# Kernel optimization log

Hardware: AMD Instinct MI355X
Metric: run time of the kernel (lower is better)

Reference implementation:

```python
import jax, jax.numpy as jnp
import numpy as np


def setup_inputs() -> dict:
    key = jax.random.key(0)
    ks = jax.random.split(key, 8)
    B, L, D, N, DM = 2, 2048, 2048, 8, 1024
    return {
        "x": jax.random.normal(ks[0], (B, L, D), jnp.float32),
        "A_log": jax.random.normal(ks[1], (D, N), jnp.float32),
        "x_proj_w": jax.random.normal(ks[2], (2 * N, D), jnp.float32) * (D ** -0.5),
        "x_proj_b": jax.random.normal(ks[3], (2 * N,), jnp.float32) * 0.02,
        "dt_proj_w": jax.random.normal(ks[4], (D, D), jnp.float32) * (D ** -0.5),
        "dt_proj_b": jax.random.normal(ks[5], (D,), jnp.float32) * 0.02,
        "out_proj_w": jax.random.normal(ks[6], (DM, D), jnp.float32) * (D ** -0.5),
        "out_proj_b": jax.random.normal(ks[7], (DM,), jnp.float32) * 0.02,
    }


def reference(x, A_log, x_proj_w, x_proj_b, dt_proj_w, dt_proj_b, out_proj_w, out_proj_b):
    # x: (B, L, D);  A_log: (D, N)
    A = -jnp.exp(A_log)                                   # (D, N), negative -> stable decay
    x_dbl = x @ x_proj_w.T + x_proj_b                     # (B, L, 2N): per-token B_t, C_t
    Bm, Cm = jnp.split(x_dbl, 2, axis=-1)                 # each (B, L, N)
    dt = jax.nn.softplus(x @ dt_proj_w.T + dt_proj_b)     # (B, L, D) selective timestep

    Bsz, L, D = x.shape
    N = A_log.shape[1]

    def step(h, inp):
        dt_t, B_t, C_t, x_t = inp                         # (B,D),(B,N),(B,N),(B,D)
        dA = jnp.exp(dt_t[..., None] * A)                 # (B, D, N)
        dB = dt_t[..., None] * B_t[:, None, :]            # (B, D, N)
        h = dA * h + dB * x_t[..., None]                  # (B, D, N)
        y = jnp.einsum("bdn,bn->bd", h, C_t)              # (B, D)
        return h, y

    h0 = jnp.zeros((Bsz, D, N), x.dtype)
    xs = (dt.transpose(1, 0, 2), Bm.transpose(1, 0, 2),
          Cm.transpose(1, 0, 2), x.transpose(1, 0, 2))
    _, ys = jax.lax.scan(step, h0, xs)                    # ys: (L, B, D)
    y = ys.transpose(1, 0, 2)                             # (B, L, D)
    return y @ out_proj_w.T + out_proj_b                  # (B, L, d_model)
```

## Files before the change

### kernel.cpp

```cpp
#include <hip/hip_runtime.h>
#include <hip/hip_bf16.h>

constexpr int Bsz = 2;
constexpr int L   = 2048;
constexpr int D   = 2048;
constexpr int Nst = 8;
constexpr int DM  = 1024;
constexpr int M   = Bsz * L;

constexpr int CH  = 64;
constexpr int T   = L / CH;
constexpr int BDN = Bsz * D * Nst;

typedef __bf16 bf16x8 __attribute__((ext_vector_type(8)));
typedef float f32x4 __attribute__((ext_vector_type(4)));

__global__ void cvt_f32_bf16(const float* __restrict__ in, __bf16* __restrict__ out, int n4) {
    int i = blockIdx.x * blockDim.x + threadIdx.x;
    if (i >= n4) return;
    float4 v = reinterpret_cast<const float4*>(in)[i];
    union { __bf16 b[4]; ushort4 u; } cv;
    cv.b[0] = (__bf16)v.x; cv.b[1] = (__bf16)v.y; cv.b[2] = (__bf16)v.z; cv.b[3] = (__bf16)v.w;
    reinterpret_cast<ushort4*>(out)[i] = cv.u;
}

__global__ __launch_bounds__(256) void xdbl_kernel(
    const float* __restrict__ x, const float* __restrict__ w,
    const float* __restrict__ bias, float* __restrict__ xdbl,
    __bf16* __restrict__ x_bf)
{
    __shared__ float sw[16 * 2048];
    const int tid = threadIdx.x;
    for (int i = tid; i < 16 * 2048 / 4; i += 256)
        reinterpret_cast<float4*>(sw)[i] = reinterpret_cast<const float4*>(w)[i];
    __syncthreads();

    const int lane = tid & 63;
    const int wrow = tid >> 6;
    for (int rr = 0; rr < 4; ++rr) {
        const int row = blockIdx.x * 16 + wrow * 4 + rr;
        const float* xr = x + (size_t)row * D;
        __bf16* xb = x_bf + (size_t)row * D;
        float acc[16];
#pragma unroll
        for (int j = 0; j < 16; ++j) acc[j] = 0.f;
        for (int k = lane * 4; k < D; k += 256) {
            float4 xv = *reinterpret_cast<const float4*>(&xr[k]);
            union { __bf16 b[4]; ushort4 u; } cv;
            cv.b[0] = (__bf16)xv.x; cv.b[1] = (__bf16)xv.y;
            cv.b[2] = (__bf16)xv.z; cv.b[3] = (__bf16)xv.w;
            *reinterpret_cast<ushort4*>(&xb[k]) = cv.u;
#pragma unroll
            for (int j = 0; j < 16; ++j) {
                float4 wv = *reinterpret_cast<const float4*>(&sw[j * D + k]);
                acc[j] += xv.x * wv.x + xv.y * wv.y + xv.z * wv.z + xv.w * wv.w;
            }
        }
#pragma unroll
        for (int j = 0; j < 16; ++j) {
            float v = acc[j];
#pragma unroll
            for (int off = 32; off > 0; off >>= 1) v += __shfl_down(v, off, 64);
            if (lane == 0) xdbl[(size_t)row * 16 + j] = v + bias[j];
        }
    }
}

__device__ inline void async16(__bf16* lds, const __bf16* g) {
    __builtin_amdgcn_global_load_lds(
        (const __attribute__((address_space(1))) void*)g,
        (__attribute__((address_space(3))) void*)lds, 16, 0, 0);
}

template <int MODE>
__global__ __launch_bounds__(256, 2) void gemm_bt(
    const __bf16* __restrict__ A, const __bf16* __restrict__ Bw,
    const float* __restrict__ bias, float* __restrict__ C,
    int N, int K)
{
    constexpr int BM = 128, BN = 128, BK = 64;
    const int NT = K / BK;
    __shared__ __attribute__((aligned(16))) __bf16 lds[2][2][BM * BK];

    const int tid  = threadIdx.x;
    const int lane = tid & 63;
    const int wid  = tid >> 6;
    const int wm   = wid >> 1, wn = wid & 1;
    const int rowBase = blockIdx.y * BM;
    const int colBase = blockIdx.x * BN;
    const int lrow = lane & 15;
    const int kgrp = lane >> 4;

    float bv[4];
#pragma unroll
    for (int n = 0; n < 4; ++n) bv[n] = bias[colBase + wn * 64 + n * 16 + lrow];
    asm volatile("s_waitcnt vmcnt(0)" ::: "memory");

    const int trow = tid >> 3;
    const int scol = ((tid & 7) ^ (trow & 7)) * 8;
    const __bf16* gA[4]; const __bf16* gB[4];
#pragma unroll
    for (int ro = 0; ro < 4; ++ro) {
        gA[ro] = A  + (size_t)(rowBase + ro * 32 + trow) * K + scol;
        gB[ro] = Bw + (size_t)(colBase + ro * 32 + trow) * K + scol;
    }

    f32x4 acc[4][4];
#pragma unroll
    for (int i = 0; i < 4; ++i)
#pragma unroll
        for (int j = 0; j < 4; ++j) acc[i][j] = f32x4{0.f, 0.f, 0.f, 0.f};

    auto stage = [&](int kt, int bsel) {
        const int k0 = kt * BK;
#pragma unroll
        for (int ro = 0; ro < 4; ++ro) {
            async16(&lds[bsel][0][ro * 2048 + tid * 8], gA[ro] + k0);
            async16(&lds[bsel][1][ro * 2048 + tid * 8], gB[ro] + k0);
        }
    };

    stage(0, 0);
    stage(1, 1);

    for (int t = 0; t < NT; ++t) {
        if (t == NT - 1) asm volatile("s_waitcnt vmcnt(0)" ::: "memory");
        else             asm volatile("s_waitcnt vmcnt(8)" ::: "memory");
        __builtin_amdgcn_s_barrier();

        const int cur = t & 1;
        bf16x8 af[4][2], bfr[4][2];
#pragma unroll
        for (int m = 0; m < 4; ++m) {
            const int row = wm * 64 + m * 16 + lrow;
#pragma unroll
            for (int kk = 0; kk < 2; ++kk) {
                const int slot = (kk * 4 + kgrp) ^ (lrow & 7);
                af[m][kk] = *reinterpret_cast<const bf16x8*>(&lds[cur][0][row * 64 + slot * 8]);
            }
        }
#pragma unroll
        for (int n = 0; n < 4; ++n) {
            const int row = wn * 64 + n * 16 + lrow;
#pragma unroll
            for (int kk = 0; kk < 2; ++kk) {
                const int slot = (kk * 4 + kgrp) ^ (lrow & 7);
                bfr[n][kk] = *reinterpret_cast<const bf16x8*>(&lds[cur][1][row * 64 + slot * 8]);
            }
        }
        asm volatile("s_waitcnt lgkmcnt(0)" ::: "memory");
        __builtin_amdgcn_sched_barrier(0);
        __builtin_amdgcn_s_barrier();

        if (t + 2 < NT) stage(t + 2, cur);

        __builtin_amdgcn_s_setprio(1);
#pragma unroll
        for (int kk = 0; kk < 2; ++kk)
#pragma unroll
            for (int m = 0; m < 4; ++m)
#pragma unroll
                for (int n = 0; n < 4; ++n)
                    acc[m][n] = __builtin_amdgcn_mfma_f32_16x16x32_bf16(af[m][kk], bfr[n][kk], acc[m][n], 0, 0, 0);
        __builtin_amdgcn_s_setprio(0);
    }

#pragma unroll
    for (int m = 0; m < 4; ++m) {
        const int row = rowBase + wm * 64 + m * 16 + kgrp * 4;
#pragma unroll
        for (int n = 0; n < 4; ++n) {
            const int col = colBase + wn * 64 + n * 16 + lrow;
#pragma unroll
            for (int r = 0; r < 4; ++r) {
                float v = acc[m][n][r] + bv[n];
                if (MODE == 1) v = (v > 20.f) ? v : log1pf(expf(v));
                C[(size_t)(row + r) * N + col] = v;
            }
        }
    }
}

__global__ __launch_bounds__(64) void scan_p1(
    const float* __restrict__ dt, const float* __restrict__ x,
    const float* __restrict__ xdbl, const float* __restrict__ A_log,
    float* __restrict__ P, float* __restrict__ Hloc)
{
    const int tid = threadIdx.x;
    int blk = blockIdx.x;
    const int c  = blk % CH;  blk /= CH;
    const int dg = blk % (D / 64);
    const int b  = blk / (D / 64);
    const int d  = dg * 64 + tid;

    float A[Nst], h[Nst], p[Nst];
#pragma unroll
    for (int n = 0; n < Nst; ++n) {
        A[n] = -expf(A_log[(size_t)d * Nst + n]);
        h[n] = 0.f; p[n] = 1.f;
    }

    __shared__ __attribute__((aligned(16))) float sBC[T * 16];
    const float4* src = reinterpret_cast<const float4*>(xdbl + ((size_t)b * L + c * T) * 16);
#pragma unroll
    for (int i = tid; i < T * 4; i += 64)
        reinterpret_cast<float4*>(sBC)[i] = src[i];
    __syncthreads();

    const float* dt_p = dt + ((size_t)b * L + c * T) * D + d;
    const float* x_p  = x  + ((size_t)b * L + c * T) * D + d;
#pragma unroll 4
    for (int t2 = 0; t2 < T; ++t2) {
        const float dtv = dt_p[(size_t)t2 * D];
        const float xv  = x_p[(size_t)t2 * D];
        const float dtx = dtv * xv;
        const float* bc = &sBC[t2 * 16];
#pragma unroll
        for (int n = 0; n < Nst; ++n) {
            const float dA = __expf(dtv * A[n]);
            p[n] *= dA;
            h[n] = dA * h[n] + dtx * bc[n];
        }
    }
    const size_t base = ((size_t)c * Bsz * D + (size_t)b * D + d) * Nst;
#pragma unroll
    for (int n = 0; n < Nst; ++n) { P[base + n] = p[n]; Hloc[base + n] = h[n]; }
}

__global__ __launch_bounds__(256) void scan_p2(
    const float* __restrict__ P, const float* __restrict__ Hloc,
    float* __restrict__ Hstart)
{
    const int id = blockIdx.x * blockDim.x + threadIdx.x;
    if (id >= BDN) return;
    float h = 0.f;
    for (int c = 0; c < CH; ++c) {
        const size_t o = (size_t)c * BDN + id;
        Hstart[o] = h;
        h = P[o] * h + Hloc[o];
    }
}

__global__ __launch_bounds__(64) void scan_p3(
    const float* __restrict__ dt, const float* __restrict__ x,
    const float* __restrict__ xdbl, const float* __restrict__ A_log,
    const float* __restrict__ Hstart, __bf16* __restrict__ y_bf)
{
    const int tid = threadIdx.x;
    int blk = blockIdx.x;
    const int c  = blk % CH;  blk /= CH;
    const int dg = blk % (D / 64);
    const int b  = blk / (D / 64);
    const int d  = dg * 64 + tid;

    float A[Nst], h[Nst];
    const size_t hbase = ((size_t)c * Bsz * D + (size_t)b * D + d) * Nst;
#pragma unroll
    for (int n = 0; n < Nst; ++n) {
        A[n] = -expf(A_log[(size_t)d * Nst + n]);
        h[n] = Hstart[hbase + n];
    }

    __shared__ __attribute__((aligned(16))) float sBC[T * 16];
    const float4* src = reinterpret_cast<const float4*>(xdbl + ((size_t)b * L + c * T) * 16);
#pragma unroll
    for (int i = tid; i < T * 4; i += 64)
        reinterpret_cast<float4*>(sBC)[i] = src[i];
    __syncthreads();

    const float* dt_p = dt + ((size_t)b * L + c * T) * D + d;
    const float* x_p  = x  + ((size_t)b * L + c * T) * D + d;
    __bf16*      y_p  = y_bf + ((size_t)b * L + c * T) * D + d;
#pragma unroll 4
    for (int t2 = 0; t2 < T; ++t2) {
        const float dtv = dt_p[(size_t)t2 * D];
        const float xv  = x_p[(size_t)t2 * D];
        const float dtx = dtv * xv;
        const float* bc = &sBC[t2 * 16];
        float y = 0.f;
#pragma unroll
        for (int n = 0; n < Nst; ++n) {
            const float dA = __expf(dtv * A[n]);
            h[n] = dA * h[n] + dtx * bc[n];
            y = fmaf(h[n], bc[8 + n], y);
        }
        y_p[(size_t)t2 * D] = (__bf16)y;
    }
}

extern "C" void kernel_launch(void* const* d_in, const int* in_sizes, int n_in,
                              void* d_out, int out_size, void* d_ws, size_t ws_size,
                              hipStream_t stream) {
    const float* x     = (const float*)d_in[0];
    const float* A_log = (const float*)d_in[1];
    const float* xpw   = (const float*)d_in[2];
    const float* xpb   = (const float*)d_in[3];
    const float* dtw   = (const float*)d_in[4];
    const float* dtb   = (const float*)d_in[5];
    const float* ow    = (const float*)d_in[6];
    const float* ob    = (const float*)d_in[7];
    float* out = (float*)d_out;

    char* ws = (char*)d_ws;
    __bf16* x_bf   = (__bf16*)(ws);
    __bf16* dtw_bf = (__bf16*)(ws + 16777216);
    __bf16* ow_bf  = (__bf16*)(ws + 25165824);
    float*  xdbl   = (float* )(ws + 29360128);
    float*  dtbuf  = (float* )(ws + 29622272);
    __bf16* y_bf   = (__bf16*)(ws + 63176704);
    float*  P      = (float*)(ws);
    float*  Hloc   = (float*)(ws + 8388608);
    float*  Hstart = (float*)(ws + 16777216);

    cvt_f32_bf16<<<(D * D / 4 + 255) / 256, 256, 0, stream>>>(dtw, dtw_bf, D * D / 4);
    cvt_f32_bf16<<<(DM * D / 4 + 255) / 256, 256, 0, stream>>>(ow, ow_bf, DM * D / 4);

    xdbl_kernel<<<M / 16, 256, 0, stream>>>(x, xpw, xpb, xdbl, x_bf);

    gemm_bt<1><<<dim3(D / 128, M / 128), 256, 0, stream>>>(x_bf, dtw_bf, dtb, dtbuf, D, D);

    const int scan_blocks = Bsz * (D / 64) * CH;
    scan_p1<<<scan_blocks, 64, 0, stream>>>(dtbuf, x, xdbl, A_log, P, Hloc);
    scan_p2<<<(BDN + 255) / 256, 256, 0, stream>>>(P, Hloc, Hstart);
    scan_p3<<<scan_blocks, 64, 0, stream>>>(dtbuf, x, xdbl, A_log, Hstart, y_bf);

    gemm_bt<0><<<dim3(DM / 128, M / 128), 256, 0, stream>>>(y_bf, ow_bf, ob, out, DM, D);
}
```

Before: 185.8 us.

## Switch GEMM to 32x32x16 MFMA and split-K the output projection

Replaces the 16x16x32 bf16 MFMA tiles in the shared GEMM with 32x32x16 tiles, which changes the LDS fragment loads and the epilogue row mapping. The output projection GEMM (only 256 blocks) is also split along K into two z-slices that accumulate with atomic adds into a zero-initialised output, with the bias added only by the first slice. This aims to cut instruction-issue overhead and to fill more CUs for the small GEMM. In exchange it adds a memset, atomic traffic, and a summation order that is no longer deterministic.

```diff
diff --git a/kernel.cpp b/kernel.cpp
--- a/kernel.cpp
+++ b/kernel.cpp
@@ -13,7 +13,8 @@
 constexpr int BDN = Bsz * D * Nst;
 
 typedef __bf16 bf16x8 __attribute__((ext_vector_type(8)));
-typedef float f32x4 __attribute__((ext_vector_type(4)));
+typedef float f32x4  __attribute__((ext_vector_type(4)));
+typedef float f32x16 __attribute__((ext_vector_type(16)));
 
 __global__ void cvt_f32_bf16(const float* __restrict__ in, __bf16* __restrict__ out, int n4) {
     int i = blockIdx.x * blockDim.x + threadIdx.x;
@@ -76,10 +77,11 @@
 __global__ __launch_bounds__(256, 2) void gemm_bt(
     const __bf16* __restrict__ A, const __bf16* __restrict__ Bw,
     const float* __restrict__ bias, float* __restrict__ C,
-    int N, int K)
+    int N, int Kfull, int Ksub)
 {
     constexpr int BM = 128, BN = 128, BK = 64;
-    const int NT = K / BK;
+    const int NT  = Ksub / BK;
+    const int zoff = blockIdx.z * Ksub;
     __shared__ __attribute__((aligned(16))) __bf16 lds[2][2][BM * BK];
 
     const int tid  = threadIdx.x;
@@ -88,12 +90,16 @@
     const int wm   = wid >> 1, wn = wid & 1;
     const int rowBase = blockIdx.y * BM;
     const int colBase = blockIdx.x * BN;
-    const int lrow = lane & 15;
-    const int kgrp = lane >> 4;
-
-    float bv[4];
-#pragma unroll
-    for (int n = 0; n < 4; ++n) bv[n] = bias[colBase + wn * 64 + n * 16 + lrow];
+    const int l31   = lane & 31;
+    const int khalf = lane >> 5;
+    const int l7    = lane & 7;
+
+    float bv[2];
+#pragma unroll
+    for (int n = 0; n < 2; ++n) {
+        bv[n] = bias[colBase + wn * 64 + n * 32 + l31];
+        if (MODE == 2 && blockIdx.z != 0) bv[n] = 0.f;
+    }
     asm volatile("s_waitcnt vmcnt(0)" ::: "memory");
 
     const int trow = tid >> 3;
@@ -101,15 +107,17 @@
     const __bf16* gA[4]; const __bf16* gB[4];
 #pragma unroll
     for (int ro = 0; ro < 4; ++ro) {
-        gA[ro] = A  + (size_t)(rowBase + ro * 32 + trow) * K + scol;
-        gB[ro] = Bw + (size_t)(colBase + ro * 32 + trow) * K + scol;
-    }
-
-    f32x4 acc[4][4];
-#pragma unroll
-    for (int i = 0; i < 4; ++i)
-#pragma unroll
-        for (int j = 0; j < 4; ++j) acc[i][j] = f32x4{0.f, 0.f, 0.f, 0.f};
+        gA[ro] = A  + (size_t)(rowBase + ro * 32 + trow) * Kfull + zoff + scol;
+        gB[ro] = Bw + (size_t)(colBase + ro * 32 + trow) * Kfull + zoff + scol;
+    }
+
+    f32x16 acc[2][2];
+#pragma unroll
+    for (int i = 0; i < 2; ++i)
+#pragma unroll
+        for (int j = 0; j < 2; ++j)
+#pragma unroll
+            for (int r = 0; r < 16; ++r) acc[i][j][r] = 0.f;
 
     auto stage = [&](int kt, int bsel) {
         const int k0 = kt * BK;
@@ -129,23 +137,23 @@
         __builtin_amdgcn_s_barrier();
 
         const int cur = t & 1;
-        bf16x8 af[4][2], bfr[4][2];
-#pragma unroll
-        for (int m = 0; m < 4; ++m) {
-            const int row = wm * 64 + m * 16 + lrow;
-#pragma unroll
-            for (int kk = 0; kk < 2; ++kk) {
-                const int slot = (kk * 4 + kgrp) ^ (lrow & 7);
-                af[m][kk] = *reinterpret_cast<const bf16x8*>(&lds[cur][0][row * 64 + slot * 8]);
+        bf16x8 af[2][4], bfr[2][4];
+#pragma unroll
+        for (int m = 0; m < 2; ++m) {
+            const int row = wm * 64 + m * 32 + l31;
+#pragma unroll
+            for (int ks = 0; ks < 4; ++ks) {
+                const int slot = (ks * 2 + khalf) ^ l7;
+                af[m][ks] = *reinterpret_cast<const bf16x8*>(&lds[cur][0][row * 64 + slot * 8]);
             }
         }
 #pragma unroll
-        for (int n = 0; n < 4; ++n) {
-            const int row = wn * 64 + n * 16 + lrow;
-#pragma unroll
-            for (int kk = 0; kk < 2; ++kk) {
-                const int slot = (kk * 4 + kgrp) ^ (lrow & 7);
-                bfr[n][kk] = *reinterpret_cast<const bf16x8*>(&lds[cur][1][row * 64 + slot * 8]);
+        for (int n = 0; n < 2; ++n) {
+            const int row = wn * 64 + n * 32 + l31;
+#pragma unroll
+            for (int ks = 0; ks < 4; ++ks) {
+                const int slot = (ks * 2 + khalf) ^ l7;
+                bfr[n][ks] = *reinterpret_cast<const bf16x8*>(&lds[cur][1][row * 64 + slot * 8]);
             }
         }
         asm volatile("s_waitcnt lgkmcnt(0)" ::: "memory");
@@ -156,26 +164,28 @@
 
         __builtin_amdgcn_s_setprio(1);
 #pragma unroll
-        for (int kk = 0; kk < 2; ++kk)
-#pragma unroll
-            for (int m = 0; m < 4; ++m)
-#pragma unroll
-                for (int n = 0; n < 4; ++n)
-                    acc[m][n] = __builtin_amdgcn_mfma_f32_16x16x32_bf16(af[m][kk], bfr[n][kk], acc[m][n], 0, 0, 0);
+        for (int ks = 0; ks < 4; ++ks)
+#pragma unroll
+            for (int m = 0; m < 2; ++m)
+#pragma unroll
+                for (int n = 0; n < 2; ++n)
+                    acc[m][n] = __builtin_amdgcn_mfma_f32_32x32x16_bf16(af[m][ks], bfr[n][ks], acc[m][n], 0, 0, 0);
         __builtin_amdgcn_s_setprio(0);
     }
 
 #pragma unroll
-    for (int m = 0; m < 4; ++m) {
-        const int row = rowBase + wm * 64 + m * 16 + kgrp * 4;
-#pragma unroll
-        for (int n = 0; n < 4; ++n) {
-            const int col = colBase + wn * 64 + n * 16 + lrow;
-#pragma unroll
-            for (int r = 0; r < 4; ++r) {
+    for (int m = 0; m < 2; ++m) {
+        const int rb = rowBase + wm * 64 + m * 32 + 4 * khalf;
+#pragma unroll
+        for (int n = 0; n < 2; ++n) {
+            const int col = colBase + wn * 64 + n * 32 + l31;
+#pragma unroll
+            for (int r = 0; r < 16; ++r) {
+                const int row = rb + (r & 3) + 8 * (r >> 2);
                 float v = acc[m][n][r] + bv[n];
                 if (MODE == 1) v = (v > 20.f) ? v : log1pf(expf(v));
-                C[(size_t)(row + r) * N + col] = v;
+                if (MODE == 2) unsafeAtomicAdd(&C[(size_t)row * N + col], v);
+                else           C[(size_t)row * N + col] = v;
             }
         }
     }
@@ -317,12 +327,13 @@
 
     xdbl_kernel<<<M / 16, 256, 0, stream>>>(x, xpw, xpb, xdbl, x_bf);
 
-    gemm_bt<1><<<dim3(D / 128, M / 128), 256, 0, stream>>>(x_bf, dtw_bf, dtb, dtbuf, D, D);
+    gemm_bt<1><<<dim3(D / 128, M / 128, 1), 256, 0, stream>>>(x_bf, dtw_bf, dtb, dtbuf, D, D, D);
 
     const int scan_blocks = Bsz * (D / 64) * CH;
     scan_p1<<<scan_blocks, 64, 0, stream>>>(dtbuf, x, xdbl, A_log, P, Hloc);
     scan_p2<<<(BDN + 255) / 256, 256, 0, stream>>>(P, Hloc, Hstart);
     scan_p3<<<scan_blocks, 64, 0, stream>>>(dtbuf, x, xdbl, A_log, Hstart, y_bf);
 
-    gemm_bt<0><<<dim3(DM / 128, M / 128), 256, 0, stream>>>(y_bf, ow_bf, ob, out, DM, D);
-}
+    hipMemsetAsync(out, 0, (size_t)out_size * sizeof(float), stream);
+    gemm_bt<2><<<dim3(DM / 128, M / 128, 2), 256, 0, stream>>>(y_bf, ow_bf, ob, out, DM, D, D / 2);
+}
```

After: 212.9 us. 1.15x slower.

## Split-K the output projection GEMM and swizzle block order in dt GEMM

Applied to the files above, without the earlier changes.

The output projection GEMM is split along K into two halves via blockIdx.z, and each half writes partial results to a workspace buffer. A new reduce kernel then sums the two partials and adds the bias. This doubles the block count for the small-N GEMM (8x32 blocks) to fill more CUs, at the cost of extra partial-result traffic and one more launch. The dt GEMM also gets an XCD-style block-index swizzle, which groups tiles to improve L2 locality across chiplets.

```diff
diff --git a/kernel.cpp b/kernel.cpp
--- a/kernel.cpp
+++ b/kernel.cpp
@@ -13,7 +13,7 @@
 constexpr int BDN = Bsz * D * Nst;
 
 typedef __bf16 bf16x8 __attribute__((ext_vector_type(8)));
-typedef float f32x4 __attribute__((ext_vector_type(4)));
+typedef float f32x4  __attribute__((ext_vector_type(4)));
 
 __global__ void cvt_f32_bf16(const float* __restrict__ in, __bf16* __restrict__ out, int n4) {
     int i = blockIdx.x * blockDim.x + threadIdx.x;
@@ -72,28 +72,38 @@
         (__attribute__((address_space(3))) void*)lds, 16, 0, 0);
 }
 
-template <int MODE>
+template <int MODE, int SWZ>
 __global__ __launch_bounds__(256, 2) void gemm_bt(
     const __bf16* __restrict__ A, const __bf16* __restrict__ Bw,
     const float* __restrict__ bias, float* __restrict__ C,
-    int N, int K)
+    int N, int Kfull, int Ksub)
 {
     constexpr int BM = 128, BN = 128, BK = 64;
-    const int NT = K / BK;
+    const int NT  = Ksub / BK;
+    const int zoff = blockIdx.z * Ksub;
     __shared__ __attribute__((aligned(16))) __bf16 lds[2][2][BM * BK];
+
+    int bx = blockIdx.x, by = blockIdx.y;
+    if (SWZ) {
+        const int lin = by * gridDim.x + bx;
+        const int cpx = (gridDim.x * gridDim.y) >> 3;
+        const int swz = (lin & 7) * cpx + (lin >> 3);
+        bx = swz % gridDim.x; by = swz / gridDim.x;
+    }
 
     const int tid  = threadIdx.x;
     const int lane = tid & 63;
     const int wid  = tid >> 6;
     const int wm   = wid >> 1, wn = wid & 1;
-    const int rowBase = blockIdx.y * BM;
-    const int colBase = blockIdx.x * BN;
+    const int rowBase = by * BM;
+    const int colBase = bx * BN;
     const int lrow = lane & 15;
     const int kgrp = lane >> 4;
 
     float bv[4];
 #pragma unroll
-    for (int n = 0; n < 4; ++n) bv[n] = bias[colBase + wn * 64 + n * 16 + lrow];
+    for (int n = 0; n < 4; ++n)
+        bv[n] = (MODE == 3) ? 0.f : bias[colBase + wn * 64 + n * 16 + lrow];
     asm volatile("s_waitcnt vmcnt(0)" ::: "memory");
 
     const int trow = tid >> 3;
@@ -101,8 +111,8 @@
     const __bf16* gA[4]; const __bf16* gB[4];
 #pragma unroll
     for (int ro = 0; ro < 4; ++ro) {
-        gA[ro] = A  + (size_t)(rowBase + ro * 32 + trow) * K + scol;
-        gB[ro] = Bw + (size_t)(colBase + ro * 32 + trow) * K + scol;
+        gA[ro] = A  + (size_t)(rowBase + ro * 32 + trow) * Kfull + zoff + scol;
+        gB[ro] = Bw + (size_t)(colBase + ro * 32 + trow) * Kfull + zoff + scol;
     }
 
     f32x4 acc[4][4];
@@ -165,6 +175,7 @@
         __builtin_amdgcn_s_setprio(0);
     }
 
+    float* Cz = (MODE == 3) ? C + (size_t)blockIdx.z * M * N : C;
 #pragma unroll
     for (int m = 0; m < 4; ++m) {
         const int row = rowBase + wm * 64 + m * 16 + kgrp * 4;
@@ -175,10 +186,26 @@
             for (int r = 0; r < 4; ++r) {
                 float v = acc[m][n][r] + bv[n];
                 if (MODE == 1) v = (v > 20.f) ? v : log1pf(expf(v));
-                C[(size_t)(row + r) * N + col] = v;
+                Cz[(size_t)(row + r) * N + col] = v;
             }
         }
     }
+}
+
+__global__ __launch_bounds__(256) void reduce_bias(
+    const float* __restrict__ part, const float* __restrict__ bias,
+    float* __restrict__ out)
+{
+    const int i = blockIdx.x * blockDim.x + threadIdx.x;
+    const int n4 = M * DM / 4;
+    if (i >= n4) return;
+    float4 a = reinterpret_cast<const float4*>(part)[i];
+    float4 b = reinterpret_cast<const float4*>(part + (size_t)M * DM)[i];
+    float4 bb = *reinterpret_cast<const float4*>(&bias[(i * 4) % DM]);
+    float4 r;
+    r.x = a.x + b.x + bb.x; r.y = a.y + b.y + bb.y;
+    r.z = a.z + b.z + bb.z; r.w = a.w + b.w + bb.w;
+    reinterpret_cast<float4*>(out)[i] = r;
 }
 
 __global__ __launch_bounds__(64) void scan_p1(
@@ -311,18 +338,20 @@
     float*  P      = (float*)(ws);
     float*  Hloc   = (float*)(ws + 8388608);
     float*  Hstart = (float*)(ws + 16777216);
+    float*  Cpart  = (float*)(ws + 29622272);
 
     cvt_f32_bf16<<<(D * D / 4 + 255) / 256, 256, 0, stream>>>(dtw, dtw_bf, D * D / 4);
     cvt_f32_bf16<<<(DM * D / 4 + 255) / 256, 256, 0, stream>>>(ow, ow_bf, DM * D / 4);
 
     xdbl_kernel<<<M / 16, 256, 0, stream>>>(x, xpw, xpb, xdbl, x_bf);
 
-    gemm_bt<1><<<dim3(D / 128, M / 128), 256, 0, stream>>>(x_bf, dtw_bf, dtb, dtbuf, D, D);
+    gemm_bt<1, 1><<<dim3(D / 128, M / 128, 1), 256, 0, stream>>>(x_bf, dtw_bf, dtb, dtbuf, D, D, D);
 
     const int scan_blocks = Bsz * (D / 64) * CH;
     scan_p1<<<scan_blocks, 64, 0, stream>>>(dtbuf, x, xdbl, A_log, P, Hloc);
     scan_p2<<<(BDN + 255) / 256, 256, 0, stream>>>(P, Hloc, Hstart);
     scan_p3<<<scan_blocks, 64, 0, stream>>>(dtbuf, x, xdbl, A_log, Hstart, y_bf);
 
-    gemm_bt<0><<<dim3(DM / 128, M / 128), 256, 0, stream>>>(y_bf, ow_bf, ob, out, DM, D);
-}
+    gemm_bt<3, 0><<<dim3(DM / 128, M / 128, 2), 256, 0, stream>>>(y_bf, ow_bf, ob, Cpart, DM, D, D / 2);
+    reduce_bias<<<(M * DM / 4 + 255) / 256, 256, 0, stream>>>(Cpart, ob, out);
+}
```

Result: slower. 197.2 us (+6.1%).
